# Kernel tuning notes

Hardware: AMD Instinct MI355X
Metric: run time of the kernel (lower is better)

Reference implementation:

```python
import jax, jax.numpy as jnp
import numpy as np

# ---- module hyper-params (match init_kwargs) ----
B, C_IN, C_OUT, K, H, W = 16, 128, 128, 3, 56, 56
M, G, STRIDE, RED = 2, 2, 1, 16
R = max(RED, C_IN // RED)            # GC_Attention bottleneck width = 16
MO = M * C_OUT                       # gc_att output channels
GROUPS = G * C_OUT                   # grouped 1x1 fc groups = 256
IN_PG = MO // GROUPS                 # in channels per group = M // G = 1
COUT_FC = C_OUT * C_IN * K * K       # generated weight elements per sample
OUT_PG = COUT_FC // GROUPS           # out channels per group = 576
PAD = K // 2
LN_EPS = 1e-5


def setup_inputs() -> dict:
    key = jax.random.key(0)
    ks = jax.random.split(key, 6)
    sc = 0.05
    return {
        "x": jax.random.normal(ks[0], (B, C_IN, H, W), jnp.float32),
        # GC_Attention: conv_mask (1x1, C->1)
        "w_mask": jax.random.normal(ks[1], (C_IN,), jnp.float32) * sc,
        "b_mask": jnp.zeros((), jnp.float32),
        # transform: conv1x1 C->R, LayerNorm(R), ReLU, conv1x1 R->M*out
        "w1": jax.random.normal(ks[2], (R, C_IN), jnp.float32) * sc,
        "b1": jnp.zeros((R,), jnp.float32),
        "ln_g": jnp.ones((R,), jnp.float32),
        "ln_b": jnp.zeros((R,), jnp.float32),
        "w2": jax.random.normal(ks[3], (MO, R), jnp.float32) * sc,
        "b2": jnp.zeros((MO,), jnp.float32),
        # fc: grouped 1x1 conv, groups=G*out, stored [groups, out_pg, in_pg]
        "w_fc": jax.random.normal(ks[4], (GROUPS, OUT_PG, IN_PG), jnp.float32) * sc,
        "b_fc": jnp.zeros((COUT_FC,), jnp.float32),
    }


def reference(x, w_mask, b_mask, w1, b1, ln_g, ln_b, w2, b2, w_fc, b_fc):
    b, c, h, w = x.shape
    # --- GC_Attention: global-context pooling via spatial softmax ---
    mask = jnp.einsum('bchw,c->bhw', x, w_mask) + b_mask        # [b,h,w]
    att = jax.nn.softmax(mask.reshape(b, -1), axis=-1)          # [b,hw]
    ctx = jnp.einsum('bcs,bs->bc', x.reshape(b, c, -1), att)    # [b,C]
    # bottleneck transform (1x1 convs on [b,*,1,1] == dense layers)
    t = ctx @ w1.T + b1                                          # [b,R]
    mu = t.mean(-1, keepdims=True)
    var = t.var(-1, keepdims=True)
    t = (t - mu) / jnp.sqrt(var + LN_EPS) * ln_g + ln_b          # LayerNorm over R
    t = jax.nn.relu(t)
    a = jax.nn.sigmoid(t @ w2.T + b2)                            # [b, M*out]
    # --- grouped 1x1 conv: generate per-sample conv weights ---
    xw = jnp.einsum('bgi,goi->bgo', a.reshape(b, GROUPS, IN_PG), w_fc)
    xw = xw.reshape(b, COUT_FC) + b_fc
    Wd = xw.reshape(b, C_OUT, C_IN, K, K)                        # per-sample kernels
    # --- per-sample conv2d (torch: groups=b on batch-folded input) ---
    def conv1(xi, wi):
        return jax.lax.conv_general_dilated(
            xi[None], wi, (STRIDE, STRIDE), [(PAD, PAD), (PAD, PAD)],
            dimension_numbers=('NCHW', 'OIHW', 'NCHW'))[0]
    return jax.vmap(conv1)(x, Wd)                                # [b, out, H, W]
```

## Files before the change

kernel.cpp:

```cpp
#include <hip/hip_runtime.h>
#include <hip/hip_bf16.h>
#include <math.h>

#define BATCH 16
#define CIN   128
#define COUT  128
#define SS    3136
#define XT_ROW 8192
#define XT_PER_B (58*XT_ROW)
#define NKB   18

typedef __attribute__((ext_vector_type(8))) __bf16 bf16x8;
typedef __attribute__((ext_vector_type(4))) float  floatx4;

static __device__ __forceinline__ unsigned short f2bf(float f) {
  union { float f; unsigned u; } v; v.f = f;
  unsigned r = v.u + 0x7fffu + ((v.u >> 16) & 1u);
  return (unsigned short)(r >> 16);
}
static __device__ __forceinline__ float bf2f(unsigned short u) {
  union { unsigned u; float f; } v; v.u = ((unsigned)u) << 16; return v.f;
}

static __device__ __forceinline__ float waveReduceSum(float v) {
  #pragma unroll
  for (int off = 32; off > 0; off >>= 1) v += __shfl_xor(v, off, 64);
  return v;
}

static __device__ __forceinline__ void load_lds16(const void* g, void* l) {
  __builtin_amdgcn_global_load_lds(
      (const __attribute__((address_space(1))) void*)g,
      (__attribute__((address_space(3))) void*)l, 16, 0, 0);
}

__global__ void k0_padT(const float* __restrict__ x, const float* __restrict__ w_mask,
                        const float* __restrict__ b_mask,
                        unsigned short* __restrict__ xT, float* __restrict__ rowsum,
                        float* __restrict__ pctx) {
  int b = blockIdx.y, prow = blockIdx.x, t = threadIdx.x;
  int y = prow - 1;
  __shared__ unsigned short sx[128 * 58];
  __shared__ float swm[128];
  __shared__ float red[4 * 56];
  __shared__ float se[56];
  bool rowvalid = ((unsigned)y < 56u);
  if (t < 128) swm[t] = w_mask[t];
  if (rowvalid) {
    int ci = t >> 1, h = t & 1;
    const float* src = x + (size_t)(b * 128 + ci) * SS + y * 56 + h * 28;
    #pragma unroll
    for (int c = 0; c < 28; c++) sx[ci * 58 + h * 28 + c] = f2bf(src[c]);
  } else {
    for (int i = t; i < 128 * 58; i += 256) sx[i] = 0;
  }
  __syncthreads();
  if (rowvalid && t < 224) {
    int xx = t % 56, g = t / 56;
    float acc = 0.f;
    #pragma unroll
    for (int k = 0; k < 32; k++) {
      int ci = g * 32 + k;
      acc += bf2f(sx[ci * 58 + xx]) * swm[ci];
    }
    red[g * 56 + xx] = acc;
  }
  __syncthreads();
  float e = 0.f;
  if (rowvalid && t < 56) {
    float m = red[t] + red[56 + t] + red[112 + t] + red[168 + t] + b_mask[0];
    e = expf(m);
    se[t] = e;
  }
  if (t < 64) {
    float s = waveReduceSum(e);
    if (t == 0) rowsum[b * 58 + prow] = s;
  }
  __syncthreads();
  {
    int c = t >> 1, h = t & 1;
    float acc = 0.f;
    if (rowvalid) {
      #pragma unroll
      for (int j = 0; j < 28; j++)
        acc += bf2f(sx[c * 58 + h * 28 + j]) * se[h * 28 + j];
    }
    acc += __shfl_xor(acc, 1, 64);
    if (h == 0) pctx[(size_t)(b * 58 + prow) * 128 + c] = acc;
  }
  int pcol = t >> 2, cig = t & 3;
  int xx = pcol - 1;
  bool colv = rowvalid && ((unsigned)xx < 56u);
  unsigned short tmp[32];
  #pragma unroll
  for (int i = 0; i < 32; i++)
    tmp[i] = colv ? sx[(cig * 32 + i) * 58 + xx] : (unsigned short)0;
  unsigned short* dst = xT + ((size_t)(b * 58 + prow) * 64 + pcol) * 128 + cig * 32;
  #pragma unroll
  for (int q = 0; q < 4; q++)
    *reinterpret_cast<uint4*>(dst + q * 8) = *reinterpret_cast<const uint4*>(tmp + q * 8);
}

__global__ void k5_gen(const float* __restrict__ rowsum, const float* __restrict__ pctx,
                       const float* __restrict__ w1, const float* __restrict__ b1,
                       const float* __restrict__ ln_g, const float* __restrict__ ln_b,
                       const float* __restrict__ w2, const float* __restrict__ b2,
                       const float* __restrict__ w_fc, const float* __restrict__ b_fc,
                       unsigned short* __restrict__ wd) {
  int co = blockIdx.x, b = blockIdx.y, t = threadIdx.x;
  __shared__ float sc[128], st[16], sn[16], sa[2], shz;
  float rv = (t < 58) ? rowsum[b * 58 + t] : 0.f;
  float acc = 0.f;
  #pragma unroll
  for (int r = 0; r < 58; r++) acc += pctx[(size_t)(b * 58 + r) * 128 + t];
  if (t < 64) {
    float z = waveReduceSum(rv);
    if (t == 0) shz = 1.0f / z;
  }
  __syncthreads();
  sc[t] = acc * shz;
  __syncthreads();
  if (t < 16) {
    float s = b1[t];
    #pragma unroll 8
    for (int c = 0; c < 128; c++) s += sc[c] * w1[t * 128 + c];
    st[t] = s;
  }
  __syncthreads();
  float mu = 0.f, m2 = 0.f;
  #pragma unroll
  for (int r = 0; r < 16; r++) { float v = st[r]; mu += v; m2 += v * v; }
  mu *= (1.f / 16.f); m2 *= (1.f / 16.f);
  float rstd = rsqrtf(m2 - mu * mu + 1e-5f);
  if (t < 16) {
    float v = (st[t] - mu) * rstd * ln_g[t] + ln_b[t];
    sn[t] = fmaxf(v, 0.f);
  }
  __syncthreads();
  if (t < 2) {
    int mo = 2 * co + t;
    float s = b2[mo];
    #pragma unroll
    for (int r = 0; r < 16; r++) s += sn[r] * w2[mo * 16 + r];
    sa[t] = 1.f / (1.f + expf(-s));
  }
  __syncthreads();
  float a0 = sa[0], a1 = sa[1];
  const float* wrow = w_fc + co * 1152;
  const float* brow = b_fc + co * 1152;
  unsigned short* drow = wd + (size_t)(b * 128 + co) * 1152;
  #pragma unroll
  for (int r = 0; r < 9; r++) {
    int e = t + 128 * r;
    int ci = e / 9, khw = e - (e / 9) * 9;
    float v = (ci < 64 ? a0 : a1) * wrow[e] + brow[e];
    int kb = khw * 2 + (ci >> 6);
    int kq = ci & 63;
    int pos = (((kq >> 3) ^ (co & 7)) << 3) | (kq & 7);
    drow[kb * 64 + pos] = f2bf(v);
  }
}

__global__ __launch_bounds__(512, 4) void k6_conv(const unsigned short* __restrict__ xT,
                                                  const unsigned short* __restrict__ wd,
                                                  float* __restrict__ out) {
  __shared__ __align__(16) unsigned short As[8192];
  __shared__ __align__(16) unsigned short Bs[8192];
  int t = threadIdx.x;
  int b = blockIdx.y, y0 = blockIdx.x * 2;
  int wave = t >> 6, lane = t & 63, l15 = lane & 15, quad = lane >> 4;
  int x7 = lane & 7;
  const unsigned short* wp  = wd + (size_t)b * (128 * 1152);
  const unsigned short* xTb = xT + (size_t)b * XT_PER_B;

  int ch0 = wave * 128 + lane, ch1 = ch0 + 64;
  int offA0 = (ch0 >> 3) * 1152 + (ch0 & 7) * 8;
  int offA1 = (ch1 >> 3) * 1152 + (ch1 & 7) * 8;
  int s0 = ch0 >> 3, s1 = ch1 >> 3;
  int c_ = lane & 7;
  int sr0 = s0 / 56, sc0 = s0 - sr0 * 56; if (sr0 >= 2) { sr0 = 0; sc0 = 0; }
  int sr1 = s1 / 56, sc1 = s1 - sr1 * 56; if (sr1 >= 2) { sr1 = 0; sc1 = 0; }
  int offB0 = (y0 + sr0) * XT_ROW + sc0 * 128 + (c_ ^ (s0 & 7)) * 8;
  int offB1 = (y0 + sr1) * XT_ROW + sc1 * 128 + (c_ ^ (s1 & 7)) * 8;
  unsigned short* dA0 = &As[wave * 1024];
  unsigned short* dA1 = &As[wave * 1024 + 512];
  unsigned short* dB0 = &Bs[wave * 1024];
  unsigned short* dB1 = &Bs[wave * 1024 + 512];

  int s_base = (wave & 3) * 32;
  int co_b   = (wave >> 2) * 64;

  floatx4 acc[4][2];
  floatx4 zero = {0.f, 0.f, 0.f, 0.f};
  #pragma unroll
  for (int i = 0; i < 4; i++)
    #pragma unroll
    for (int j = 0; j < 2; j++) acc[i][j] = zero;

  for (int kb = 0; kb < NKB; kb++) {
    int khw = kb >> 1;
    int kh = khw / 3;
    int kw = khw - kh * 3;
    int dB = kh * XT_ROW + kw * 128 + ((kb & 1) << 6);
    int dA = kb * 64;
    __syncthreads();
    load_lds16(wp + offA0 + dA, dA0);
    load_lds16(wp + offA1 + dA, dA1);
    load_lds16(xTb + offB0 + dB, dB0);
    load_lds16(xTb + offB1 + dB, dB1);
    __syncthreads();
    #pragma unroll
    for (int kk = 0; kk < 2; kk++) {
      bf16x8 af[4], bfr[2];
      int pc = ((kk * 4 + quad) ^ x7) << 3;
      #pragma unroll
      for (int i = 0; i < 4; i++)
        af[i] = *reinterpret_cast<const bf16x8*>(&As[(co_b + i * 16 + l15) * 64 + pc]);
      #pragma unroll
      for (int j = 0; j < 2; j++)
        bfr[j] = *reinterpret_cast<const bf16x8*>(&Bs[(s_base + j * 16 + l15) * 64 + pc]);
      #pragma unroll
      for (int i = 0; i < 4; i++)
        #pragma unroll
        for (int j = 0; j < 2; j++)
          acc[i][j] = __builtin_amdgcn_mfma_f32_16x16x32_bf16(af[i], bfr[j], acc[i][j], 0, 0, 0);
    }
  }

  float* ob = out + (size_t)b * COUT * SS + y0 * 56;
  #pragma unroll
  for (int i = 0; i < 4; i++) {
    #pragma unroll
    for (int j = 0; j < 2; j++) {
      int sl = s_base + j * 16 + l15;
      if (sl < 112) {
        int row = (sl >= 56) ? 1 : 0;
        int col = sl - row * 56;
        #pragma unroll
        for (int r = 0; r < 4; r++) {
          int co = co_b + i * 16 + quad * 4 + r;
          ob[(size_t)co * SS + row * 56 + col] = acc[i][j][r];
        }
      }
    }
  }
}

extern "C" void kernel_launch(void* const* d_in, const int* in_sizes, int n_in,
                              void* d_out, int out_size, void* d_ws, size_t ws_size,
                              hipStream_t stream) {
  const float* x      = (const float*)d_in[0];
  const float* w_mask = (const float*)d_in[1];
  const float* b_mask = (const float*)d_in[2];
  const float* w1     = (const float*)d_in[3];
  const float* b1     = (const float*)d_in[4];
  const float* ln_g   = (const float*)d_in[5];
  const float* ln_b   = (const float*)d_in[6];
  const float* w2     = (const float*)d_in[7];
  const float* b2     = (const float*)d_in[8];
  const float* w_fc   = (const float*)d_in[9];
  const float* b_fc   = (const float*)d_in[10];
  float* out = (float*)d_out;

  char* ws = (char*)d_ws;
  unsigned short* xT  = (unsigned short*)(ws);
  unsigned short* wdw = (unsigned short*)(ws + 15204352);
  float* rowsum = (float*)(ws + 19922944);
  float* pctx   = (float*)(ws + 19927040);

  k0_padT<<<dim3(58, 16),  dim3(256), 0, stream>>>(x, w_mask, b_mask, xT, rowsum, pctx);
  k5_gen <<<dim3(128, 16), dim3(128), 0, stream>>>(rowsum, pctx, w1, b1, ln_g, ln_b,
                                                   w2, b2, w_fc, b_fc, wdw);
  k6_conv<<<dim3(28, 16),  dim3(512), 0, stream>>>(xT, wdw, out);
}
```

Baseline: 134.7 us.

## Vectorize x staging, early-exit pad rows, split MLP from weight generation

The pad/transpose kernel now loads x with float4 reads into a swizzled 64-wide LDS layout, and padding rows take an early exit that only writes zeros. The former per-(co,b) generation kernel recomputed the whole context reduction and MLP 2048 times. It is split into a 16-block MLP kernel that writes the sigmoid gates into the pctx buffer, plus a weight-generation kernel that stages bf16 weights in LDS for coalesced 16-byte stores. This adds one kernel launch, reuses pctx as scratch after it has been reduced, and changes the LDS swizzle pattern, which could cause bank conflicts if it is wrong.

```diff
diff --git a/kernel.cpp b/kernel.cpp
--- a/kernel.cpp
+++ b/kernel.cpp
@@ -34,40 +34,63 @@
       (__attribute__((address_space(3))) void*)l, 16, 0, 0);
 }
 
-__global__ void k0_padT(const float* __restrict__ x, const float* __restrict__ w_mask,
-                        const float* __restrict__ b_mask,
-                        unsigned short* __restrict__ xT, float* __restrict__ rowsum,
-                        float* __restrict__ pctx) {
+static __device__ __forceinline__ int sswz(int ci) {
+  return (ci ^ (ci >> 4)) & 15;
+}
+
+__global__ __launch_bounds__(256, 4)
+void k0_padT(const float* __restrict__ x, const float* __restrict__ w_mask,
+             const float* __restrict__ b_mask,
+             unsigned short* __restrict__ xT, float* __restrict__ rowsum,
+             float* __restrict__ pctx) {
   int b = blockIdx.y, prow = blockIdx.x, t = threadIdx.x;
   int y = prow - 1;
-  __shared__ unsigned short sx[128 * 58];
+  __shared__ __align__(16) unsigned short sx[128 * 64];
   __shared__ float swm[128];
   __shared__ float red[4 * 56];
   __shared__ float se[56];
   bool rowvalid = ((unsigned)y < 56u);
+
+  if (!rowvalid) {
+    unsigned short* dst = xT + (size_t)(b * 58 + prow) * XT_ROW;
+    uint4 z4 = make_uint4(0u, 0u, 0u, 0u);
+    #pragma unroll
+    for (int q = 0; q < 4; q++)
+      *reinterpret_cast<uint4*>(dst + (size_t)(t + 256 * q) * 8) = z4;
+    if (t == 0) rowsum[b * 58 + prow] = 0.f;
+    if (t < 128) pctx[(size_t)(b * 58 + prow) * 128 + t] = 0.f;
+    return;
+  }
+
   if (t < 128) swm[t] = w_mask[t];
-  if (rowvalid) {
-    int ci = t >> 1, h = t & 1;
-    const float* src = x + (size_t)(b * 128 + ci) * SS + y * 56 + h * 28;
-    #pragma unroll
-    for (int c = 0; c < 28; c++) sx[ci * 58 + h * 28 + c] = f2bf(src[c]);
-  } else {
-    for (int i = t; i < 128 * 58; i += 256) sx[i] = 0;
-  }
-  __syncthreads();
-  if (rowvalid && t < 224) {
+  #pragma unroll
+  for (int i = 0; i < 7; i++) {
+    int c = t + 256 * i;
+    int ci = c / 14, j = c - ci * 14;
+    const float4 v = *reinterpret_cast<const float4*>(
+        x + (size_t)(b * 128 + ci) * SS + y * 56 + j * 4);
+    union { unsigned short s[4]; uint2 u; } pk;
+    pk.s[0] = f2bf(v.x); pk.s[1] = f2bf(v.y);
+    pk.s[2] = f2bf(v.z); pk.s[3] = f2bf(v.w);
+    int blk = j ^ sswz(ci);
+    *reinterpret_cast<uint2*>(&sx[ci * 64 + (blk << 2)]) = pk.u;
+  }
+  __syncthreads();
+
+  if (t < 224) {
     int xx = t % 56, g = t / 56;
     float acc = 0.f;
     #pragma unroll
     for (int k = 0; k < 32; k++) {
       int ci = g * 32 + k;
-      acc += bf2f(sx[ci * 58 + xx]) * swm[ci];
+      acc += bf2f(sx[ci * 64 + ((((xx >> 2) ^ sswz(ci)) << 2) | (xx & 3))]) * swm[ci];
     }
     red[g * 56 + xx] = acc;
   }
   __syncthreads();
+
   float e = 0.f;
-  if (rowvalid && t < 56) {
+  if (t < 56) {
     float m = red[t] + red[56 + t] + red[112 + t] + red[168 + t] + b_mask[0];
     e = expf(m);
     se[t] = e;
@@ -76,39 +99,44 @@
     float s = waveReduceSum(e);
     if (t == 0) rowsum[b * 58 + prow] = s;
   }
-  __syncthreads();
+
+  {
+    int pcol = t >> 2, cig = t & 3;
+    int xx = pcol - 1;
+    bool colv = ((unsigned)xx < 56u);
+    unsigned short tmp[32];
+    #pragma unroll
+    for (int i = 0; i < 32; i++) {
+      int ci = cig * 32 + i;
+      tmp[i] = colv ? sx[ci * 64 + ((((xx >> 2) ^ sswz(ci)) << 2) | (xx & 3))]
+                    : (unsigned short)0;
+    }
+    unsigned short* dst = xT + ((size_t)(b * 58 + prow) * 64 + pcol) * 128 + cig * 32;
+    #pragma unroll
+    for (int q = 0; q < 4; q++)
+      *reinterpret_cast<uint4*>(dst + q * 8) = *reinterpret_cast<const uint4*>(tmp + q * 8);
+  }
+  __syncthreads();
+
   {
     int c = t >> 1, h = t & 1;
     float acc = 0.f;
-    if (rowvalid) {
-      #pragma unroll
-      for (int j = 0; j < 28; j++)
-        acc += bf2f(sx[c * 58 + h * 28 + j]) * se[h * 28 + j];
+    #pragma unroll
+    for (int j = 0; j < 28; j++) {
+      int col = h * 28 + j;
+      acc += bf2f(sx[c * 64 + ((((col >> 2) ^ sswz(c)) << 2) | (col & 3))]) * se[col];
     }
     acc += __shfl_xor(acc, 1, 64);
     if (h == 0) pctx[(size_t)(b * 58 + prow) * 128 + c] = acc;
   }
-  int pcol = t >> 2, cig = t & 3;
-  int xx = pcol - 1;
-  bool colv = rowvalid && ((unsigned)xx < 56u);
-  unsigned short tmp[32];
-  #pragma unroll
-  for (int i = 0; i < 32; i++)
-    tmp[i] = colv ? sx[(cig * 32 + i) * 58 + xx] : (unsigned short)0;
-  unsigned short* dst = xT + ((size_t)(b * 58 + prow) * 64 + pcol) * 128 + cig * 32;
-  #pragma unroll
-  for (int q = 0; q < 4; q++)
-    *reinterpret_cast<uint4*>(dst + q * 8) = *reinterpret_cast<const uint4*>(tmp + q * 8);
-}
-
-__global__ void k5_gen(const float* __restrict__ rowsum, const float* __restrict__ pctx,
+}
+
+__global__ void k4_mlp(const float* __restrict__ rowsum, float* __restrict__ pctx,
                        const float* __restrict__ w1, const float* __restrict__ b1,
                        const float* __restrict__ ln_g, const float* __restrict__ ln_b,
-                       const float* __restrict__ w2, const float* __restrict__ b2,
-                       const float* __restrict__ w_fc, const float* __restrict__ b_fc,
-                       unsigned short* __restrict__ wd) {
-  int co = blockIdx.x, b = blockIdx.y, t = threadIdx.x;
-  __shared__ float sc[128], st[16], sn[16], sa[2], shz;
+                       const float* __restrict__ w2, const float* __restrict__ b2) {
+  int b = blockIdx.x, t = threadIdx.x;
+  __shared__ float sc[128], st[16], sn[16], shz;
   float rv = (t < 58) ? rowsum[b * 58 + t] : 0.f;
   float acc = 0.f;
   #pragma unroll
@@ -127,37 +155,47 @@
     st[t] = s;
   }
   __syncthreads();
-  float mu = 0.f, m2 = 0.f;
-  #pragma unroll
-  for (int r = 0; r < 16; r++) { float v = st[r]; mu += v; m2 += v * v; }
-  mu *= (1.f / 16.f); m2 *= (1.f / 16.f);
-  float rstd = rsqrtf(m2 - mu * mu + 1e-5f);
   if (t < 16) {
+    float mu = 0.f, m2 = 0.f;
+    #pragma unroll
+    for (int r = 0; r < 16; r++) { float v = st[r]; mu += v; m2 += v * v; }
+    mu *= (1.f / 16.f); m2 *= (1.f / 16.f);
+    float rstd = rsqrtf(m2 - mu * mu + 1e-5f);
     float v = (st[t] - mu) * rstd * ln_g[t] + ln_b[t];
     sn[t] = fmaxf(v, 0.f);
   }
   __syncthreads();
-  if (t < 2) {
-    int mo = 2 * co + t;
+  #pragma unroll
+  for (int k = 0; k < 2; k++) {
+    int mo = t + 128 * k;
     float s = b2[mo];
     #pragma unroll
     for (int r = 0; r < 16; r++) s += sn[r] * w2[mo * 16 + r];
-    sa[t] = 1.f / (1.f + expf(-s));
-  }
-  __syncthreads();
-  float a0 = sa[0], a1 = sa[1];
-  const float* wrow = w_fc + co * 1152;
-  const float* brow = b_fc + co * 1152;
-  unsigned short* drow = wd + (size_t)(b * 128 + co) * 1152;
-  #pragma unroll
-  for (int r = 0; r < 9; r++) {
-    int e = t + 128 * r;
-    int ci = e / 9, khw = e - (e / 9) * 9;
-    float v = (ci < 64 ? a0 : a1) * wrow[e] + brow[e];
-    int kb = khw * 2 + (ci >> 6);
-    int kq = ci & 63;
-    int pos = (((kq >> 3) ^ (co & 7)) << 3) | (kq & 7);
-    drow[kb * 64 + pos] = f2bf(v);
+    pctx[(size_t)b * (58 * 128) + mo] = 1.f / (1.f + expf(-s));
+  }
+}
+
+__global__ void k5_wgen(const float* __restrict__ w_fc, const float* __restrict__ b_fc,
+                        const float* __restrict__ abuf, unsigned short* __restrict__ wd) {
+  int co = blockIdx.x, bp = blockIdx.y, t = threadIdx.x;
+  int ci = t & 127, bb = t >> 7, b = bp * 2 + bb;
+  __shared__ unsigned short sw[2][1152];
+  const float* wr = w_fc + co * 1152 + ci * 9;
+  const float* br = b_fc + co * 1152 + ci * 9;
+  float a = abuf[(size_t)b * (58 * 128) + 2 * co + (ci >> 6)];
+  int kq = ci & 63;
+  int pos = (((kq >> 3) ^ (co & 7)) << 3) | (kq & 7);
+  int kb0 = ci >> 6;
+  #pragma unroll
+  for (int khw = 0; khw < 9; khw++) {
+    float v = a * wr[khw] + br[khw];
+    sw[bb][(khw * 2 + kb0) * 64 + pos] = f2bf(v);
+  }
+  __syncthreads();
+  for (int c = t; c < 288; c += 256) {
+    int row = c / 144, q = c - row * 144;
+    unsigned short* dst = wd + (size_t)((bp * 2 + row) * 128 + co) * 1152 + q * 8;
+    *reinterpret_cast<uint4*>(dst) = *reinterpret_cast<const uint4*>(&sw[row][q * 8]);
   }
 }
 
@@ -269,7 +307,7 @@
   float* pctx   = (float*)(ws + 19927040);
 
   k0_padT<<<dim3(58, 16),  dim3(256), 0, stream>>>(x, w_mask, b_mask, xT, rowsum, pctx);
-  k5_gen <<<dim3(128, 16), dim3(128), 0, stream>>>(rowsum, pctx, w1, b1, ln_g, ln_b,
-                                                   w2, b2, w_fc, b_fc, wdw);
+  k4_mlp <<<dim3(16),      dim3(128), 0, stream>>>(rowsum, pctx, w1, b1, ln_g, ln_b, w2, b2);
+  k5_wgen<<<dim3(128, 8),  dim3(256), 0, stream>>>(w_fc, b_fc, pctx, wdw);
   k6_conv<<<dim3(28, 16),  dim3(512), 0, stream>>>(xT, wdw, out);
 }
```

Result: no change. 132.7 us (-1.4%).
